# Performance work log

Measured on AMD Instinct MI355X. Metric: run time of the kernel, lower is better.

The kernel has to match this reference:

```python
import jax, jax.numpy as jnp
import numpy as np

B, T, C = 2, 2048, 1024
N_HEAD = 16
HEAD_DIM = C // N_HEAD

def setup_inputs() -> dict:
    key = jax.random.key(0)
    k1, k2, k3 = jax.random.split(key, 3)
    x = jax.random.normal(k1, (B, T, C), dtype=jnp.float32)
    # Dense kernel init scale ~ 1/sqrt(fan_in) for stable softmax
    w_attn = jax.random.normal(k2, (C, 3 * C), dtype=jnp.float32) / np.sqrt(C)
    w_proj = jax.random.normal(k3, (C, C), dtype=jnp.float32) / np.sqrt(C)
    return {"x": x, "w_attn": w_attn, "w_proj": w_proj}

def reference(x, w_attn, w_proj):
    Bc, Tc, Cc = x.shape
    # QKV projection (use_bias=False)
    qkv = x @ w_attn  # [B, T, 3C]
    q, k, v = jnp.split(qkv, 3, axis=-1)
    # [B, T, C] -> [B, H, T, D]
    def heads(a):
        return a.reshape(Bc, Tc, N_HEAD, HEAD_DIM).swapaxes(1, 2)
    q, k, v = heads(q), heads(k), heads(v)
    scale = 1.0 / jnp.sqrt(jnp.asarray(HEAD_DIM, dtype=x.dtype))
    attn = jnp.einsum('bhqd,bhkd->bhqk', q, k) * scale  # [B, H, T, T]
    attn = jax.nn.softmax(attn, axis=-1)
    # dropout=0.0 / deterministic -> identity
    y = jnp.einsum('bhqk,bhkd->bhqd', attn, v)  # [B, H, T, D]
    y = y.swapaxes(1, 2).reshape(Bc, Tc, Cc)
    return y @ w_proj  # output projection, no bias, dropout identity
```

## Files before the change

### kernel.cpp

```cpp
#include <hip/hip_runtime.h>
#include <hip/hip_bf16.h>

#define B_   2
#define T_   2048
#define C_   1024
#define NH_  16
#define HD_  64

typedef __attribute__((ext_vector_type(8))) short short8;
typedef __attribute__((ext_vector_type(4))) float float4_;
typedef __attribute__((ext_vector_type(4))) _Float16 half4_;
typedef __attribute__((ext_vector_type(2))) __fp16  fp16x2;
typedef __attribute__((ext_vector_type(4))) unsigned short ushort4_;

static __device__ __forceinline__ unsigned short f2bf(float f) {
    union { float f; unsigned u; } v; v.f = f;
    unsigned r = v.u + 0x7fffu + ((v.u >> 16) & 1u);
    return (unsigned short)(r >> 16);
}

static __device__ __forceinline__ void g2l16(const void* g, void* l) {
    __builtin_amdgcn_global_load_lds(
        (const __attribute__((address_space(1))) void*)g,
        (__attribute__((address_space(3))) void*)l, 16, 0, 0);
}

__global__ __launch_bounds__(256) void prep(
    const float* __restrict__ x,      unsigned short* __restrict__ xb,
    const float* __restrict__ wA,     unsigned short* __restrict__ wTa,
    const float* __restrict__ wP,     unsigned short* __restrict__ wTp)
{
    const int t = threadIdx.x;
    int blk = blockIdx.x;
    if (blk < 2048) {
        int i = blk * 256 + t;
        const float4* p = (const float4*)x + (size_t)i * 2;
        float4 a = p[0], b = p[1];
        short8 o;
        o[0]=f2bf(a.x); o[1]=f2bf(a.y); o[2]=f2bf(a.z); o[3]=f2bf(a.w);
        o[4]=f2bf(b.x); o[5]=f2bf(b.y); o[6]=f2bf(b.z); o[7]=f2bf(b.w);
        *((short8*)xb + i) = o;
        return;
    }
    blk -= 2048;
    const float* in; unsigned short* out; int Cc;
    if (blk < 16 * 48) { in = wA; out = wTa; Cc = 3072; }
    else               { blk -= 16 * 48; in = wP; out = wTp; Cc = 1024; }
    const int r0 = (blk % 16) * 64, c0 = (blk / 16) * 64;
    const int R = 1024;
    __shared__ __align__(16) unsigned short Ts[64][72];
    #pragma unroll
    for (int cc = 0; cc < 2; ++cc) {
        int c = cc * 256 + t;
        int r = c >> 3, col = (c & 7) * 8;
        const float* p = in + (size_t)(r0 + r) * Cc + c0 + col;
        #pragma unroll
        for (int i = 0; i < 8; ++i) Ts[col + i][r] = f2bf(p[i]);
    }
    __syncthreads();
    #pragma unroll
    for (int cc = 0; cc < 2; ++cc) {
        int c = cc * 256 + t;
        int cr = c >> 3, oc = (c & 7) * 8;
        uint4 v = *(const uint4*)(&Ts[cr][oc]);
        *(uint4*)(out + (size_t)(c0 + cr) * R + r0 + oc) = v;
    }
}

template <bool C_F32, int BM, bool WRITE_VT>
__global__ __launch_bounds__(256) void gemm_bt(
    const unsigned short* __restrict__ A,
    const unsigned short* __restrict__ Bt,
    void* __restrict__ Cv, unsigned short* __restrict__ vt,
    int M, int N, int K)
{
    __shared__ __align__(16) unsigned short As[BM * 32];
    __shared__ __align__(16) unsigned short Bs[128 * 32];
    const int t = threadIdx.x, lane = t & 63, w = t >> 6;
    const int quad = lane >> 4, ln = lane & 15;

    const int nwg  = gridDim.x * gridDim.y;
    const int flat = blockIdx.y * gridDim.x + blockIdx.x;
    const int q8   = nwg >> 3;
    const int swz  = (flat & 7) * q8 + (flat >> 3);
    const int bm = swz % gridDim.x, bn = swz / gridDim.x;

    constexpr int NI = (BM == 128) ? 4 : 2;
    const int mw = (BM == 128) ? (w & 1) * 64 : 0;
    const int nw = (BM == 128) ? (w >> 1) * 64 : w * 32;
    float4_ acc[4][NI] = {};

    constexpr int AROWS = BM / 4;
    const unsigned short* Ag = A  + (size_t)(bm * BM + w * AROWS + (lane >> 2)) * K + (lane & 3) * 8;
    const unsigned short* Bg = Bt + (size_t)(bn * 128 + w * 32 + (lane >> 2)) * K + (lane & 3) * 8;
    unsigned short* lA = &As[(w * AROWS) * 32 + lane * 8];
    unsigned short* lB = &Bs[(w * 32) * 32 + lane * 8];

    for (int k0 = 0; k0 < K; k0 += 32) {
        g2l16(Ag + k0, lA);
        if (BM == 128) g2l16(Ag + (size_t)16 * K + k0, lA + 16 * 32);
        g2l16(Bg + k0,                  lB);
        g2l16(Bg + (size_t)16 * K + k0, lB + 16 * 32);
        __syncthreads();
        short8 a[4], b[NI];
        #pragma unroll
        for (int i = 0; i < 4; ++i)
            a[i] = *(const short8*)(&As[(mw + i * 16 + ln) * 32 + quad * 8]);
        #pragma unroll
        for (int i = 0; i < NI; ++i)
            b[i] = *(const short8*)(&Bs[(nw + i * 16 + ln) * 32 + quad * 8]);
        #pragma unroll
        for (int mi = 0; mi < 4; ++mi)
            #pragma unroll
            for (int ni = 0; ni < NI; ++ni)
                acc[mi][ni] = __builtin_amdgcn_mfma_f32_16x16x32_bf16(
                    a[mi], b[ni], acc[mi][ni], 0, 0, 0);
        __syncthreads();
    }

    const int row0 = bm * BM + mw + quad * 4;
    const int col0 = bn * 128 + nw + ln;
    #pragma unroll
    for (int mi = 0; mi < 4; ++mi)
        #pragma unroll
        for (int ni = 0; ni < NI; ++ni) {
            #pragma unroll
            for (int i = 0; i < 4; ++i) {
                size_t idx = (size_t)(row0 + mi * 16 + i) * N + col0 + ni * 16;
                if (C_F32) ((float*)Cv)[idx] = acc[mi][ni][i];
                else       ((unsigned short*)Cv)[idx] = f2bf(acc[mi][ni][i]);
            }
            if (WRITE_VT && col0 + ni * 16 >= 2 * C_) {
                int d     = col0 + ni * 16 - 2 * C_;
                int token = row0 + mi * 16;
                int b     = token >> 11, tloc = token & 2047;
                union { fp16x2 h2[2]; ushort4_ u4; } pk;
                pk.h2[0] = __builtin_amdgcn_cvt_pkrtz(acc[mi][ni][0], acc[mi][ni][1]);
                pk.h2[1] = __builtin_amdgcn_cvt_pkrtz(acc[mi][ni][2], acc[mi][ni][3]);
                *(ushort4_*)(vt + ((size_t)b * 1024 + d) * T_ + tloc) = pk.u4;
            }
        }
}

__global__ __launch_bounds__(256) void attn(
    const unsigned short* __restrict__ qkv,
    const unsigned short* __restrict__ vt,
    unsigned short* __restrict__ Y)
{
    __shared__ __align__(16) unsigned short Qs[128][72];
    __shared__ __align__(16) unsigned short Ks[64][72];
    __shared__ __align__(16) unsigned short Vs[64][72];

    const int t = threadIdx.x;
    const int qt = blockIdx.x, bh = blockIdx.y;
    const int b = bh >> 4, h = bh & 15;
    const int lane = t & 63, w = t >> 6;
    const int quad = lane >> 4, ln = lane & 15;

    const unsigned short* Qg  = qkv + (size_t)b * T_ * (3 * C_) + (size_t)h * HD_;
    const unsigned short* Kg  = Qg + C_;
    const unsigned short* Vtg = vt + (size_t)bh * HD_ * T_;

    #pragma unroll
    for (int cc = 0; cc < 4; ++cc) {
        int c = cc * 256 + t;
        int r = c >> 3, col = (c & 7) * 8;
        *(uint4*)(&Qs[r][col]) = *(const uint4*)(Qg + (size_t)(qt * 128 + r) * (3 * C_) + col);
    }

    const int r0 = t >> 3, c0v = (t & 7) * 8;
    const int r1 = r0 + 32;
    const int vsw = r0 & 8;

    uint4 kr0 = *(const uint4*)(Kg + (size_t)r0 * (3 * C_) + c0v);
    uint4 kr1 = *(const uint4*)(Kg + (size_t)r1 * (3 * C_) + c0v);
    uint4 vr0 = *(const uint4*)(Vtg + (size_t)r0 * T_ + c0v);
    uint4 vr1 = *(const uint4*)(Vtg + (size_t)r1 * T_ + c0v);

    __syncthreads();

    short8 qf[2][2];
    #pragma unroll
    for (int qm = 0; qm < 2; ++qm)
        #pragma unroll
        for (int dh = 0; dh < 2; ++dh)
            qf[qm][dh] = *(const short8*)(&Qs[w * 32 + qm * 16 + ln][dh * 32 + quad * 8]);

    float4_ ot[4][2] = {};
    float ls[2] = {0.f, 0.f};
    const float C1 = 0.125f * 1.44269504f;
    const float C2 = 8.0f * 1.44269504f;

    for (int kt = 0; kt < T_ / 64; ++kt) {
        if (kt) __syncthreads();
        *(uint4*)(&Ks[r0][c0v]) = kr0;
        *(uint4*)(&Ks[r1][c0v]) = kr1;
        {
            uint4 v0 = vr0, v1 = vr1;
            if (vsw) {
                uint4 s;
                s.x = v0.z; s.y = v0.w; s.z = v0.x; s.w = v0.y; v0 = s;
                s.x = v1.z; s.y = v1.w; s.z = v1.x; s.w = v1.y; v1 = s;
            }
            *(uint4*)(&Vs[r0][c0v]) = v0;
            *(uint4*)(&Vs[r1][c0v]) = v1;
        }
        __syncthreads();

        if (kt + 1 < T_ / 64) {
            int kb = (kt + 1) * 64;
            kr0 = *(const uint4*)(Kg + (size_t)(kb + r0) * (3 * C_) + c0v);
            kr1 = *(const uint4*)(Kg + (size_t)(kb + r1) * (3 * C_) + c0v);
            vr0 = *(const uint4*)(Vtg + (size_t)r0 * T_ + kb + c0v);
            vr1 = *(const uint4*)(Vtg + (size_t)r1 * T_ + kb + c0v);
        }

        half4_ pf[4][2];
        #pragma unroll
        for (int ct = 0; ct < 4; ++ct) {
            short8 kb0 = *(const short8*)(&Ks[ct * 16 + ln][quad * 8]);
            short8 kb1 = *(const short8*)(&Ks[ct * 16 + ln][32 + quad * 8]);
            #pragma unroll
            for (int qm = 0; qm < 2; ++qm) {
                float4_ st = {};
                st = __builtin_amdgcn_mfma_f32_16x16x32_bf16(kb0, qf[qm][0], st, 0, 0, 0);
                st = __builtin_amdgcn_mfma_f32_16x16x32_bf16(kb1, qf[qm][1], st, 0, 0, 0);
                float p0 = __builtin_amdgcn_exp2f(st[0] * C1 - C2);
                float p1 = __builtin_amdgcn_exp2f(st[1] * C1 - C2);
                float p2 = __builtin_amdgcn_exp2f(st[2] * C1 - C2);
                float p3 = __builtin_amdgcn_exp2f(st[3] * C1 - C2);
                ls[qm] += (p0 + p1) + (p2 + p3);
                union { fp16x2 h2[2]; half4_ h4; } u;
                u.h2[0] = __builtin_amdgcn_cvt_pkrtz(p0, p1);
                u.h2[1] = __builtin_amdgcn_cvt_pkrtz(p2, p3);
                pf[ct][qm] = u.h4;
            }
        }

        const char* vbase = (const char*)(&Vs[0][0]);
        const int rsw = ln & 8;
        #pragma unroll
        for (int dt = 0; dt < 4; ++dt) {
            int roff = (dt * 16 + ln) * 144;
            #pragma unroll
            for (int ct = 0; ct < 4; ++ct) {
                half4_ va = *(const half4_*)(vbase + roff + ((ct * 32 + quad * 8) ^ rsw));
                #pragma unroll
                for (int qm = 0; qm < 2; ++qm)
                    ot[dt][qm] = __builtin_amdgcn_mfma_f32_16x16x16f16(
                        va, pf[ct][qm], ot[dt][qm], 0, 0, 0);
            }
        }
    }

    #pragma unroll
    for (int qm = 0; qm < 2; ++qm) {
        ls[qm] += __shfl_xor(ls[qm], 16, 64);
        ls[qm] += __shfl_xor(ls[qm], 32, 64);
    }

    #pragma unroll
    for (int qm = 0; qm < 2; ++qm) {
        unsigned short* Yr = Y + ((size_t)b * T_ + qt * 128 + w * 32 + qm * 16 + ln) * C_ + h * HD_;
        float inv = 1.0f / ls[qm];
        #pragma unroll
        for (int dt = 0; dt < 4; ++dt)
            #pragma unroll
            for (int i = 0; i < 4; ++i)
                Yr[dt * 16 + quad * 4 + i] = f2bf(ot[dt][qm][i] * inv);
    }
}

extern "C" void kernel_launch(void* const* d_in, const int* in_sizes, int n_in,
                              void* d_out, int out_size, void* d_ws, size_t ws_size,
                              hipStream_t stream)
{
    const float* x      = (const float*)d_in[0];
    const float* w_attn = (const float*)d_in[1];
    const float* w_proj = (const float*)d_in[2];
    float* out = (float*)d_out;

    unsigned short* qkv = (unsigned short*)d_ws;
    unsigned short* y   = qkv + (size_t)4096 * 3072;
    unsigned short* wTa = y   + (size_t)4096 * 1024;
    unsigned short* wTp = wTa + (size_t)3072 * 1024;
    unsigned short* vt  = wTp + (size_t)1024 * 1024;
    unsigned short* xb  = y;

    prep<<<2048 + 16 * 48 + 16 * 16, 256, 0, stream>>>(x, xb, w_attn, wTa, w_proj, wTp);

    gemm_bt<false, 128, true><<<dim3(32, 24), 256, 0, stream>>>(
        xb, wTa, qkv, vt, 4096, 3072, 1024);
    attn<<<dim3(16, 32), 256, 0, stream>>>(qkv, vt, y);
    gemm_bt<true, 64, false><<<dim3(64, 8), 256, 0, stream>>>(
        y, wTp, out, nullptr, 4096, 1024, 1024);
}
```

Measured before the change: 206.2 us.

## Double-buffer K/V tiles in attention and drop GEMM block swizzle

The attention loop now keeps two LDS buffers for K and V. Each tile is stored into the alternate buffer while the current one is being computed, which cuts the two barriers per tile to one and overlaps global loads further ahead. The GEMM kernel also drops its XCD-style block-index swizzle and uses plain blockIdx mapping, which may hurt L2 locality on multi-XCD hardware. The cost is extra LDS and more live registers for the second prefetch set, which could lower occupancy.

```diff
diff --git a/kernel.cpp b/kernel.cpp
--- a/kernel.cpp
+++ b/kernel.cpp
@@ -78,13 +78,7 @@
     __shared__ __align__(16) unsigned short Bs[128 * 32];
     const int t = threadIdx.x, lane = t & 63, w = t >> 6;
     const int quad = lane >> 4, ln = lane & 15;
-
-    const int nwg  = gridDim.x * gridDim.y;
-    const int flat = blockIdx.y * gridDim.x + blockIdx.x;
-    const int q8   = nwg >> 3;
-    const int swz  = (flat & 7) * q8 + (flat >> 3);
-    const int bm = swz % gridDim.x, bn = swz / gridDim.x;
-
+    const int bm = blockIdx.x, bn = blockIdx.y;
     constexpr int NI = (BM == 128) ? 4 : 2;
     const int mw = (BM == 128) ? (w & 1) * 64 : 0;
     const int nw = (BM == 128) ? (w >> 1) * 64 : w * 32;
@@ -142,14 +136,58 @@
         }
 }
 
+__device__ __forceinline__ void attn_tile(
+    const unsigned short (*Ksb)[72], const unsigned short (*Vsb)[72],
+    const short8 (&qf)[2][2], float4_ (&ot)[4][2], float (&ls)[2],
+    int quad, int ln)
+{
+    const float C1 = 0.125f * 1.44269504f;
+    const float C2 = 8.0f * 1.44269504f;
+    half4_ pf[4][2];
+    #pragma unroll
+    for (int ct = 0; ct < 4; ++ct) {
+        short8 kb0 = *(const short8*)(&Ksb[ct * 16 + ln][quad * 8]);
+        short8 kb1 = *(const short8*)(&Ksb[ct * 16 + ln][32 + quad * 8]);
+        #pragma unroll
+        for (int qm = 0; qm < 2; ++qm) {
+            float4_ st = {};
+            st = __builtin_amdgcn_mfma_f32_16x16x32_bf16(kb0, qf[qm][0], st, 0, 0, 0);
+            st = __builtin_amdgcn_mfma_f32_16x16x32_bf16(kb1, qf[qm][1], st, 0, 0, 0);
+            float p0 = __builtin_amdgcn_exp2f(st[0] * C1 - C2);
+            float p1 = __builtin_amdgcn_exp2f(st[1] * C1 - C2);
+            float p2 = __builtin_amdgcn_exp2f(st[2] * C1 - C2);
+            float p3 = __builtin_amdgcn_exp2f(st[3] * C1 - C2);
+            ls[qm] += (p0 + p1) + (p2 + p3);
+            union { fp16x2 h2[2]; half4_ h4; } u;
+            u.h2[0] = __builtin_amdgcn_cvt_pkrtz(p0, p1);
+            u.h2[1] = __builtin_amdgcn_cvt_pkrtz(p2, p3);
+            pf[ct][qm] = u.h4;
+        }
+    }
+    const char* vbase = (const char*)(&Vsb[0][0]);
+    const int rsw = ln & 8;
+    #pragma unroll
+    for (int dt = 0; dt < 4; ++dt) {
+        int roff = (dt * 16 + ln) * 144;
+        #pragma unroll
+        for (int ct = 0; ct < 4; ++ct) {
+            half4_ va = *(const half4_*)(vbase + roff + ((ct * 32 + quad * 8) ^ rsw));
+            #pragma unroll
+            for (int qm = 0; qm < 2; ++qm)
+                ot[dt][qm] = __builtin_amdgcn_mfma_f32_16x16x16f16(
+                    va, pf[ct][qm], ot[dt][qm], 0, 0, 0);
+        }
+    }
+}
+
 __global__ __launch_bounds__(256) void attn(
     const unsigned short* __restrict__ qkv,
     const unsigned short* __restrict__ vt,
     unsigned short* __restrict__ Y)
 {
     __shared__ __align__(16) unsigned short Qs[128][72];
-    __shared__ __align__(16) unsigned short Ks[64][72];
-    __shared__ __align__(16) unsigned short Vs[64][72];
+    __shared__ __align__(16) unsigned short Ks[2][64][72];
+    __shared__ __align__(16) unsigned short Vs[2][64][72];
 
     const int t = threadIdx.x;
     const int qt = blockIdx.x, bh = blockIdx.y;
@@ -172,10 +210,27 @@
     const int r1 = r0 + 32;
     const int vsw = r0 & 8;
 
-    uint4 kr0 = *(const uint4*)(Kg + (size_t)r0 * (3 * C_) + c0v);
-    uint4 kr1 = *(const uint4*)(Kg + (size_t)r1 * (3 * C_) + c0v);
-    uint4 vr0 = *(const uint4*)(Vtg + (size_t)r0 * T_ + c0v);
-    uint4 vr1 = *(const uint4*)(Vtg + (size_t)r1 * T_ + c0v);
+    auto load_kv = [&](uint4& k0, uint4& k1, uint4& v0, uint4& v1, int kb) {
+        k0 = *(const uint4*)(Kg + (size_t)(kb + r0) * (3 * C_) + c0v);
+        k1 = *(const uint4*)(Kg + (size_t)(kb + r1) * (3 * C_) + c0v);
+        v0 = *(const uint4*)(Vtg + (size_t)r0 * T_ + kb + c0v);
+        v1 = *(const uint4*)(Vtg + (size_t)r1 * T_ + kb + c0v);
+    };
+    auto store_kv = [&](unsigned short (*Kb)[72], unsigned short (*Vb)[72],
+                        uint4 k0, uint4 k1, uint4 v0, uint4 v1) {
+        *(uint4*)(&Kb[r0][c0v]) = k0;
+        *(uint4*)(&Kb[r1][c0v]) = k1;
+        if (vsw) {
+            uint4 s;
+            s.x = v0.z; s.y = v0.w; s.z = v0.x; s.w = v0.y; v0 = s;
+            s.x = v1.z; s.y = v1.w; s.z = v1.x; s.w = v1.y; v1 = s;
+        }
+        *(uint4*)(&Vb[r0][c0v]) = v0;
+        *(uint4*)(&Vb[r1][c0v]) = v1;
+    };
+
+    uint4 ka0, ka1, va0, va1, kb0r, kb1r, vb0r, vb1r;
+    load_kv(ka0, ka1, va0, va1, 0);
 
     __syncthreads();
 
@@ -186,71 +241,24 @@
         for (int dh = 0; dh < 2; ++dh)
             qf[qm][dh] = *(const short8*)(&Qs[w * 32 + qm * 16 + ln][dh * 32 + quad * 8]);
 
+    store_kv(Ks[0], Vs[0], ka0, ka1, va0, va1);
+    load_kv(kb0r, kb1r, vb0r, vb1r, 64);
+    __syncthreads();
+
     float4_ ot[4][2] = {};
     float ls[2] = {0.f, 0.f};
-    const float C1 = 0.125f * 1.44269504f;
-    const float C2 = 8.0f * 1.44269504f;
-
-    for (int kt = 0; kt < T_ / 64; ++kt) {
-        if (kt) __syncthreads();
-        *(uint4*)(&Ks[r0][c0v]) = kr0;
-        *(uint4*)(&Ks[r1][c0v]) = kr1;
-        {
-            uint4 v0 = vr0, v1 = vr1;
-            if (vsw) {
-                uint4 s;
-                s.x = v0.z; s.y = v0.w; s.z = v0.x; s.w = v0.y; v0 = s;
-                s.x = v1.z; s.y = v1.w; s.z = v1.x; s.w = v1.y; v1 = s;
-            }
-            *(uint4*)(&Vs[r0][c0v]) = v0;
-            *(uint4*)(&Vs[r1][c0v]) = v1;
-        }
+
+    constexpr int NT = T_ / 64;
+    for (int it = 0; it < NT; it += 2) {
+        if (it + 1 < NT) store_kv(Ks[1], Vs[1], kb0r, kb1r, vb0r, vb1r);
+        if (it + 2 < NT) load_kv(ka0, ka1, va0, va1, (it + 2) * 64);
+        attn_tile(Ks[0], Vs[0], qf, ot, ls, quad, ln);
         __syncthreads();
 
-        if (kt + 1 < T_ / 64) {
-            int kb = (kt + 1) * 64;
-            kr0 = *(const uint4*)(Kg + (size_t)(kb + r0) * (3 * C_) + c0v);
-            kr1 = *(const uint4*)(Kg + (size_t)(kb + r1) * (3 * C_) + c0v);
-            vr0 = *(const uint4*)(Vtg + (size_t)r0 * T_ + kb + c0v);
-            vr1 = *(const uint4*)(Vtg + (size_t)r1 * T_ + kb + c0v);
-        }
-
-        half4_ pf[4][2];
-        #pragma unroll
-        for (int ct = 0; ct < 4; ++ct) {
-            short8 kb0 = *(const short8*)(&Ks[ct * 16 + ln][quad * 8]);
-            short8 kb1 = *(const short8*)(&Ks[ct * 16 + ln][32 + quad * 8]);
-            #pragma unroll
-            for (int qm = 0; qm < 2; ++qm) {
-                float4_ st = {};
-                st = __builtin_amdgcn_mfma_f32_16x16x32_bf16(kb0, qf[qm][0], st, 0, 0, 0);
-                st = __builtin_amdgcn_mfma_f32_16x16x32_bf16(kb1, qf[qm][1], st, 0, 0, 0);
-                float p0 = __builtin_amdgcn_exp2f(st[0] * C1 - C2);
-                float p1 = __builtin_amdgcn_exp2f(st[1] * C1 - C2);
-                float p2 = __builtin_amdgcn_exp2f(st[2] * C1 - C2);
-                float p3 = __builtin_amdgcn_exp2f(st[3] * C1 - C2);
-                ls[qm] += (p0 + p1) + (p2 + p3);
-                union { fp16x2 h2[2]; half4_ h4; } u;
-                u.h2[0] = __builtin_amdgcn_cvt_pkrtz(p0, p1);
-                u.h2[1] = __builtin_amdgcn_cvt_pkrtz(p2, p3);
-                pf[ct][qm] = u.h4;
-            }
-        }
-
-        const char* vbase = (const char*)(&Vs[0][0]);
-        const int rsw = ln & 8;
-        #pragma unroll
-        for (int dt = 0; dt < 4; ++dt) {
-            int roff = (dt * 16 + ln) * 144;
-            #pragma unroll
-            for (int ct = 0; ct < 4; ++ct) {
-                half4_ va = *(const half4_*)(vbase + roff + ((ct * 32 + quad * 8) ^ rsw));
-                #pragma unroll
-                for (int qm = 0; qm < 2; ++qm)
-                    ot[dt][qm] = __builtin_amdgcn_mfma_f32_16x16x16f16(
-                        va, pf[ct][qm], ot[dt][qm], 0, 0, 0);
-            }
-        }
+        if (it + 2 < NT) store_kv(Ks[0], Vs[0], ka0, ka1, va0, va1);
+        if (it + 3 < NT) load_kv(kb0r, kb1r, vb0r, vb1r, (it + 3) * 64);
+        if (it + 1 < NT) attn_tile(Ks[1], Vs[1], qf, ot, ls, quad, ln);
+        __syncthreads();
     }
 
     #pragma unroll
```

Result: faster. 190.0 us (-7.8%).
